# Kernel optimization log

Measured on AMD Instinct MI355X. Metric: run time of the kernel, lower is better.

Reference implementation:

```python
import jax, jax.numpy as jnp
import numpy as np

C = 128
GROUPS = 8
EPS = 1e-5


def setup_inputs() -> dict:
    key = jax.random.key(0)
    ks = jax.random.split(key, 7)
    x = jax.random.normal(ks[0], (8, C, 256, 256), dtype=jnp.float32)
    gn_w = jax.random.normal(ks[1], (C,), dtype=jnp.float32) * 0.02 + 1.0
    gn_b = jax.random.normal(ks[2], (C,), dtype=jnp.float32) * 0.02
    w1 = jax.random.normal(ks[3], (C, C), dtype=jnp.float32) * (1.0 / np.sqrt(C))
    b1 = jax.random.normal(ks[4], (C,), dtype=jnp.float32) * 0.02
    w2 = jax.random.normal(ks[5], (C, C), dtype=jnp.float32) * (1.0 / np.sqrt(C))
    b2 = jax.random.normal(ks[6], (C,), dtype=jnp.float32) * 0.02
    return {"x": x, "gn_w": gn_w, "gn_b": gn_b, "w1": w1, "b1": b1, "w2": w2, "b2": b2}


def reference(x, gn_w, gn_b, w1, b1, w2, b2):
    # fft2 -> ifft2(..).real round-trip (faithful to original; numerically ~identity)
    x_ifft = jnp.fft.ifft2(jnp.fft.fft2(x, axes=(-2, -1)), axes=(-2, -1)).real.astype(x.dtype)

    # GroupNorm over (C//G, H, W) per group
    B, Ch, H, W = x_ifft.shape
    g = x_ifft.reshape(B, GROUPS, Ch // GROUPS, H, W)
    mean = g.mean(axis=(2, 3, 4), keepdims=True)
    var = g.var(axis=(2, 3, 4), keepdims=True)
    xn = ((g - mean) * jax.lax.rsqrt(var + EPS)).reshape(B, Ch, H, W)
    xn = xn * gn_w[None, :, None, None] + gn_b[None, :, None, None]

    # 1x1 conv -> ReLU -> 1x1 conv (as channel GEMMs)
    h = jnp.einsum('oc,bchw->bohw', w1, xn) + b1[None, :, None, None]
    h = jax.nn.relu(h)
    ffn = jnp.einsum('oc,bchw->bohw', w2, h) + b2[None, :, None, None]
    return x_ifft + ffn
```

## Files before the change

### kernel.cpp

```cpp
#include <hip/hip_runtime.h>

typedef __attribute__((ext_vector_type(8))) short s16x8;
typedef __attribute__((ext_vector_type(4))) float f32x4;

#define CCH 128
#define HWSZ 65536

__device__ __forceinline__ ushort f2bf(float f) {
  uint u = __float_as_uint(f);
  u += 0x7fffu + ((u >> 16) & 1u);
  return (ushort)(u >> 16);
}

__device__ __forceinline__ int swz(int row, int col) {
  return (row << 7) | (col ^ ((row & 7) << 3));
}

__global__ __launch_bounds__(256) void prep_weights(const float* __restrict__ w1,
                                                    const float* __restrict__ w2,
                                                    ushort* __restrict__ w1b,
                                                    ushort* __restrict__ w2b) {
  int i = blockIdx.x * 256 + threadIdx.x;
  float4 a = ((const float4*)w1)[i];
  ushort4 oa;
  oa.x = f2bf(a.x); oa.y = f2bf(a.y); oa.z = f2bf(a.z); oa.w = f2bf(a.w);
  ((ushort4*)w1b)[i] = oa;
  float4 b = ((const float4*)w2)[i];
  ushort4 ob;
  ob.x = f2bf(b.x); ob.y = f2bf(b.y); ob.z = f2bf(b.z); ob.w = f2bf(b.w);
  ((ushort4*)w2b)[i] = ob;
}

__global__ __launch_bounds__(256) void stats_partial(const float* __restrict__ x,
                                                     float* __restrict__ partials) {
  const float4* xp = (const float4*)(x + ((size_t)blockIdx.x << 16));
  const int tid = threadIdx.x;
  float s1 = 0.f, s2 = 0.f;
#pragma unroll 8
  for (int i = 0; i < 64; ++i) {
    float4 v = xp[i * 256 + tid];
    s1 += v.x + v.y + v.z + v.w;
    s2 += v.x * v.x + v.y * v.y + v.z * v.z + v.w * v.w;
  }
#pragma unroll
  for (int off = 32; off > 0; off >>= 1) {
    s1 += __shfl_down(s1, off);
    s2 += __shfl_down(s2, off);
  }
  __shared__ float r1[4], r2[4];
  const int wv = tid >> 6;
  if ((tid & 63) == 0) { r1[wv] = s1; r2[wv] = s2; }
  __syncthreads();
  if (tid == 0) {
    partials[blockIdx.x * 2]     = r1[0] + r1[1] + r1[2] + r1[3];
    partials[blockIdx.x * 2 + 1] = r2[0] + r2[1] + r2[2] + r2[3];
  }
}

__global__ void stats_finalize(const float* __restrict__ partials,
                               const float* __restrict__ gn_w,
                               const float* __restrict__ gn_b,
                               float* __restrict__ scale, float* __restrict__ shift) {
  const int t = threadIdx.x;
  float s1 = 0.f, s2 = 0.f;
#pragma unroll
  for (int i = 0; i < 16; ++i) {
    s1 += partials[(t * 16 + i) * 2];
    s2 += partials[(t * 16 + i) * 2 + 1];
  }
  const float invN = 1.0f / 1048576.0f;
  const float mean = s1 * invN;
  const float var = s2 * invN - mean * mean;
  const float rstd = rsqrtf(var + 1e-5f);
  const int b = t >> 3, g = t & 7;
  for (int i = 0; i < 16; ++i) {
    const int c = g * 16 + i;
    const float sc = rstd * gn_w[c];
    scale[b * CCH + c] = sc;
    shift[b * CCH + c] = gn_b[c] - mean * sc;
  }
}

__global__ __launch_bounds__(256) void fused_main(
    const float* __restrict__ x, const ushort* __restrict__ w1b,
    const ushort* __restrict__ w2b, const float* __restrict__ scale,
    const float* __restrict__ shift, const float* __restrict__ b1,
    const float* __restrict__ b2, float* __restrict__ out) {
  __shared__ ushort sB[128 * 128];
  const int tid = threadIdx.x;
  const int b = blockIdx.x >> 9;
  const int p0 = (blockIdx.x & 511) << 7;
  const int lane = tid & 63;
  const int wv = tid >> 6;
  const int fl = lane & 15;
  const int fh = lane >> 4;

  {
    const int p = tid & 127;
    const int ch0 = (tid >> 7) << 6;
    const float* xb = x + (((size_t)b * CCH) << 16) + p0 + p;
    const float* scb = scale + b * CCH;
    const float* shb = shift + b * CCH;
#pragma unroll
    for (int cc = 0; cc < 64; cc += 16) {
      float v[16];
#pragma unroll
      for (int i = 0; i < 16; ++i)
        v[i] = xb[((size_t)(ch0 + cc + i)) << 16];
#pragma unroll
      for (int q = 0; q < 4; ++q) {
        const int c = ch0 + cc + q * 4;
        ushort4 pk;
        pk.x = f2bf(v[q * 4 + 0] * scb[c + 0] + shb[c + 0]);
        pk.y = f2bf(v[q * 4 + 1] * scb[c + 1] + shb[c + 1]);
        pk.z = f2bf(v[q * 4 + 2] * scb[c + 2] + shb[c + 2]);
        pk.w = f2bf(v[q * 4 + 3] * scb[c + 3] + shb[c + 3]);
        *(ushort4*)&sB[swz(p, c)] = pk;
      }
    }
  }
  __syncthreads();

  f32x4 acc[2][8];
#pragma unroll
  for (int f = 0; f < 2; ++f)
#pragma unroll
    for (int j = 0; j < 8; ++j)
      acc[f][j] = (f32x4){0.f, 0.f, 0.f, 0.f};

#pragma unroll
  for (int k0 = 0; k0 < 128; k0 += 32) {
    const int kb = k0 + fh * 8;
    const s16x8 a0 = *(const s16x8*)(w1b + (wv * 32 + fl) * CCH + kb);
    const s16x8 a1 = *(const s16x8*)(w1b + (wv * 32 + 16 + fl) * CCH + kb);
#pragma unroll
    for (int j = 0; j < 8; ++j) {
      const s16x8 bf = *(const s16x8*)&sB[swz(j * 16 + fl, kb)];
      acc[0][j] = __builtin_amdgcn_mfma_f32_16x16x32_bf16(a0, bf, acc[0][j], 0, 0, 0);
      acc[1][j] = __builtin_amdgcn_mfma_f32_16x16x32_bf16(a1, bf, acc[1][j], 0, 0, 0);
    }
  }
  __syncthreads();

#pragma unroll
  for (int f = 0; f < 2; ++f) {
    const int ob = wv * 32 + f * 16 + fh * 4;
    float bb[4];
#pragma unroll
    for (int r = 0; r < 4; ++r) bb[r] = b1[ob + r];
#pragma unroll
    for (int j = 0; j < 8; ++j) {
      const int pcol = j * 16 + fl;
      ushort4 pk;
      pk.x = f2bf(fmaxf(acc[f][j][0] + bb[0], 0.f));
      pk.y = f2bf(fmaxf(acc[f][j][1] + bb[1], 0.f));
      pk.z = f2bf(fmaxf(acc[f][j][2] + bb[2], 0.f));
      pk.w = f2bf(fmaxf(acc[f][j][3] + bb[3], 0.f));
      *(ushort4*)&sB[swz(pcol, ob)] = pk;
    }
  }
  __syncthreads();

  f32x4 acc2[2][8];
#pragma unroll
  for (int f = 0; f < 2; ++f)
#pragma unroll
    for (int j = 0; j < 8; ++j)
      acc2[f][j] = (f32x4){0.f, 0.f, 0.f, 0.f};

#pragma unroll
  for (int k0 = 0; k0 < 128; k0 += 32) {
    const int kb = k0 + fh * 8;
    const s16x8 a0 = *(const s16x8*)(w2b + (wv * 32 + fl) * CCH + kb);
    const s16x8 a1 = *(const s16x8*)(w2b + (wv * 32 + 16 + fl) * CCH + kb);
#pragma unroll
    for (int j = 0; j < 8; ++j) {
      const s16x8 bf = *(const s16x8*)&sB[swz(j * 16 + fl, kb)];
      acc2[0][j] = __builtin_amdgcn_mfma_f32_16x16x32_bf16(a0, bf, acc2[0][j], 0, 0, 0);
      acc2[1][j] = __builtin_amdgcn_mfma_f32_16x16x32_bf16(a1, bf, acc2[1][j], 0, 0, 0);
    }
  }

#pragma unroll
  for (int f = 0; f < 2; ++f) {
    const int ob = wv * 32 + f * 16 + fh * 4;
    float bb[4];
#pragma unroll
    for (int r = 0; r < 4; ++r) bb[r] = b2[ob + r];
#pragma unroll
    for (int j = 0; j < 8; ++j) {
      const int pcol = p0 + j * 16 + fl;
      const size_t base = (((size_t)(b * CCH + ob)) << 16) + pcol;
#pragma unroll
      for (int r = 0; r < 4; ++r) {
        const size_t idx = base + ((size_t)r << 16);
        out[idx] = x[idx] + acc2[f][j][r] + bb[r];
      }
    }
  }
}

extern "C" void kernel_launch(void* const* d_in, const int* in_sizes, int n_in,
                              void* d_out, int out_size, void* d_ws, size_t ws_size,
                              hipStream_t stream) {
  const float* x    = (const float*)d_in[0];
  const float* gn_w = (const float*)d_in[1];
  const float* gn_b = (const float*)d_in[2];
  const float* w1   = (const float*)d_in[3];
  const float* b1   = (const float*)d_in[4];
  const float* w2   = (const float*)d_in[5];
  const float* b2   = (const float*)d_in[6];
  float* out = (float*)d_out;

  char* ws = (char*)d_ws;
  float* partials = (float*)ws;
  float* scale    = (float*)(ws + 8192);
  float* shift    = (float*)(ws + 12288);
  ushort* w1b     = (ushort*)(ws + 16384);
  ushort* w2b     = (ushort*)(ws + 49152);

  hipLaunchKernelGGL(prep_weights, dim3(16), dim3(256), 0, stream, w1, w2, w1b, w2b);
  hipLaunchKernelGGL(stats_partial, dim3(1024), dim3(256), 0, stream, x, partials);
  hipLaunchKernelGGL(stats_finalize, dim3(1), dim3(64), 0, stream, partials, gn_w, gn_b, scale, shift);
  hipLaunchKernelGGL(fused_main, dim3(4096), dim3(256), 0, stream, x, w1b, w2b, scale, shift, b1, b2, out);
}
```

Before: 214.3 us.

## Fold GroupNorm affine into per-batch W1 and restructure main kernel as single-wave blocks

Folds the GroupNorm scale and shift into a per-batch bf16 copy of W1 plus a per-batch bias c1, computed by a new small kernel. The main pass then converts raw x straight to bf16 with no per-element normalize. The main kernel becomes one-wave blocks of 64 threads covering 32 pixels each, with all 128 output channels per wave, so no block barriers are needed. Tradeoffs: weights are re-read per block from global/cache with less reuse per block, there is an extra launch, and bf16 rounding now applies to raw x and scaled weights rather than normalized values.

```diff
diff --git a/kernel.cpp b/kernel.cpp
--- a/kernel.cpp
+++ b/kernel.cpp
@@ -4,7 +4,6 @@
 typedef __attribute__((ext_vector_type(4))) float f32x4;
 
 #define CCH 128
-#define HWSZ 65536
 
 __device__ __forceinline__ ushort f2bf(float f) {
   uint u = __float_as_uint(f);
@@ -16,19 +15,13 @@
   return (row << 7) | (col ^ ((row & 7) << 3));
 }
 
-__global__ __launch_bounds__(256) void prep_weights(const float* __restrict__ w1,
-                                                    const float* __restrict__ w2,
-                                                    ushort* __restrict__ w1b,
-                                                    ushort* __restrict__ w2b) {
+__global__ __launch_bounds__(256) void prep_w2(const float* __restrict__ w2,
+                                               ushort* __restrict__ w2b) {
   int i = blockIdx.x * 256 + threadIdx.x;
-  float4 a = ((const float4*)w1)[i];
-  ushort4 oa;
-  oa.x = f2bf(a.x); oa.y = f2bf(a.y); oa.z = f2bf(a.z); oa.w = f2bf(a.w);
-  ((ushort4*)w1b)[i] = oa;
-  float4 b = ((const float4*)w2)[i];
-  ushort4 ob;
-  ob.x = f2bf(b.x); ob.y = f2bf(b.y); ob.z = f2bf(b.z); ob.w = f2bf(b.w);
-  ((ushort4*)w2b)[i] = ob;
+  float4 a = ((const float4*)w2)[i];
+  ushort4 o;
+  o.x = f2bf(a.x); o.y = f2bf(a.y); o.z = f2bf(a.z); o.w = f2bf(a.w);
+  ((ushort4*)w2b)[i] = o;
 }
 
 __global__ __launch_bounds__(256) void stats_partial(const float* __restrict__ x,
@@ -81,120 +74,116 @@
   }
 }
 
-__global__ __launch_bounds__(256) void fused_main(
-    const float* __restrict__ x, const ushort* __restrict__ w1b,
-    const ushort* __restrict__ w2b, const float* __restrict__ scale,
-    const float* __restrict__ shift, const float* __restrict__ b1,
+__global__ __launch_bounds__(128) void fold_w1(const float* __restrict__ w1,
+                                               const float* __restrict__ b1,
+                                               const float* __restrict__ scale,
+                                               const float* __restrict__ shift,
+                                               ushort* __restrict__ W1b,
+                                               float* __restrict__ c1) {
+  const int b = blockIdx.x >> 7, o = blockIdx.x & 127, c = threadIdx.x;
+  const float wv = w1[o * CCH + c];
+  W1b[(b << 14) + o * CCH + c] = f2bf(wv * scale[b * CCH + c]);
+  float s = wv * shift[b * CCH + c];
+#pragma unroll
+  for (int off = 32; off > 0; off >>= 1) s += __shfl_down(s, off);
+  __shared__ float tmp[2];
+  if ((threadIdx.x & 63) == 0) tmp[threadIdx.x >> 6] = s;
+  __syncthreads();
+  if (threadIdx.x == 0) c1[(b << 7) + o] = tmp[0] + tmp[1] + b1[o];
+}
+
+__global__ __launch_bounds__(64, 3) void wave_fused(
+    const float* __restrict__ x, const ushort* __restrict__ W1b,
+    const ushort* __restrict__ w2b, const float* __restrict__ c1,
     const float* __restrict__ b2, float* __restrict__ out) {
-  __shared__ ushort sB[128 * 128];
-  const int tid = threadIdx.x;
-  const int b = blockIdx.x >> 9;
-  const int p0 = (blockIdx.x & 511) << 7;
-  const int lane = tid & 63;
-  const int wv = tid >> 6;
-  const int fl = lane & 15;
-  const int fh = lane >> 4;
+  __shared__ __align__(16) ushort sB[32 * CCH];
+  const int lane = threadIdx.x;
+  const int b = blockIdx.x >> 11;
+  const int p0 = (blockIdx.x & 2047) << 5;
+  const int fl = lane & 15, fh = lane >> 4;
 
   {
-    const int p = tid & 127;
-    const int ch0 = (tid >> 7) << 6;
+    const int p = lane & 31;
+    const int ch0 = (lane >> 5) << 6;
     const float* xb = x + (((size_t)b * CCH) << 16) + p0 + p;
-    const float* scb = scale + b * CCH;
-    const float* shb = shift + b * CCH;
-#pragma unroll
-    for (int cc = 0; cc < 64; cc += 16) {
-      float v[16];
-#pragma unroll
-      for (int i = 0; i < 16; ++i)
-        v[i] = xb[((size_t)(ch0 + cc + i)) << 16];
-#pragma unroll
-      for (int q = 0; q < 4; ++q) {
-        const int c = ch0 + cc + q * 4;
-        ushort4 pk;
-        pk.x = f2bf(v[q * 4 + 0] * scb[c + 0] + shb[c + 0]);
-        pk.y = f2bf(v[q * 4 + 1] * scb[c + 1] + shb[c + 1]);
-        pk.z = f2bf(v[q * 4 + 2] * scb[c + 2] + shb[c + 2]);
-        pk.w = f2bf(v[q * 4 + 3] * scb[c + 3] + shb[c + 3]);
-        *(ushort4*)&sB[swz(p, c)] = pk;
-      }
-    }
-  }
-  __syncthreads();
-
-  f32x4 acc[2][8];
-#pragma unroll
-  for (int f = 0; f < 2; ++f)
-#pragma unroll
-    for (int j = 0; j < 8; ++j)
-      acc[f][j] = (f32x4){0.f, 0.f, 0.f, 0.f};
-
-#pragma unroll
-  for (int k0 = 0; k0 < 128; k0 += 32) {
-    const int kb = k0 + fh * 8;
-    const s16x8 a0 = *(const s16x8*)(w1b + (wv * 32 + fl) * CCH + kb);
-    const s16x8 a1 = *(const s16x8*)(w1b + (wv * 32 + 16 + fl) * CCH + kb);
-#pragma unroll
-    for (int j = 0; j < 8; ++j) {
-      const s16x8 bf = *(const s16x8*)&sB[swz(j * 16 + fl, kb)];
-      acc[0][j] = __builtin_amdgcn_mfma_f32_16x16x32_bf16(a0, bf, acc[0][j], 0, 0, 0);
-      acc[1][j] = __builtin_amdgcn_mfma_f32_16x16x32_bf16(a1, bf, acc[1][j], 0, 0, 0);
-    }
-  }
-  __syncthreads();
-
-#pragma unroll
-  for (int f = 0; f < 2; ++f) {
-    const int ob = wv * 32 + f * 16 + fh * 4;
-    float bb[4];
-#pragma unroll
-    for (int r = 0; r < 4; ++r) bb[r] = b1[ob + r];
-#pragma unroll
-    for (int j = 0; j < 8; ++j) {
-      const int pcol = j * 16 + fl;
+#pragma unroll
+    for (int i = 0; i < 16; ++i) {
+      const int c = ch0 + i * 4;
+      const float v0 = xb[(size_t)(c + 0) << 16];
+      const float v1 = xb[(size_t)(c + 1) << 16];
+      const float v2 = xb[(size_t)(c + 2) << 16];
+      const float v3 = xb[(size_t)(c + 3) << 16];
       ushort4 pk;
-      pk.x = f2bf(fmaxf(acc[f][j][0] + bb[0], 0.f));
-      pk.y = f2bf(fmaxf(acc[f][j][1] + bb[1], 0.f));
-      pk.z = f2bf(fmaxf(acc[f][j][2] + bb[2], 0.f));
-      pk.w = f2bf(fmaxf(acc[f][j][3] + bb[3], 0.f));
-      *(ushort4*)&sB[swz(pcol, ob)] = pk;
-    }
-  }
-  __syncthreads();
-
-  f32x4 acc2[2][8];
-#pragma unroll
-  for (int f = 0; f < 2; ++f)
-#pragma unroll
-    for (int j = 0; j < 8; ++j)
-      acc2[f][j] = (f32x4){0.f, 0.f, 0.f, 0.f};
-
-#pragma unroll
-  for (int k0 = 0; k0 < 128; k0 += 32) {
-    const int kb = k0 + fh * 8;
-    const s16x8 a0 = *(const s16x8*)(w2b + (wv * 32 + fl) * CCH + kb);
-    const s16x8 a1 = *(const s16x8*)(w2b + (wv * 32 + 16 + fl) * CCH + kb);
-#pragma unroll
-    for (int j = 0; j < 8; ++j) {
-      const s16x8 bf = *(const s16x8*)&sB[swz(j * 16 + fl, kb)];
-      acc2[0][j] = __builtin_amdgcn_mfma_f32_16x16x32_bf16(a0, bf, acc2[0][j], 0, 0, 0);
-      acc2[1][j] = __builtin_amdgcn_mfma_f32_16x16x32_bf16(a1, bf, acc2[1][j], 0, 0, 0);
-    }
-  }
-
-#pragma unroll
-  for (int f = 0; f < 2; ++f) {
-    const int ob = wv * 32 + f * 16 + fh * 4;
-    float bb[4];
-#pragma unroll
-    for (int r = 0; r < 4; ++r) bb[r] = b2[ob + r];
-#pragma unroll
-    for (int j = 0; j < 8; ++j) {
-      const int pcol = p0 + j * 16 + fl;
-      const size_t base = (((size_t)(b * CCH + ob)) << 16) + pcol;
+      pk.x = f2bf(v0); pk.y = f2bf(v1); pk.z = f2bf(v2); pk.w = f2bf(v3);
+      *(ushort4*)&sB[swz(p, c)] = pk;
+    }
+  }
+
+  f32x4 acc[8][2];
+#pragma unroll
+  for (int to = 0; to < 8; ++to)
+#pragma unroll
+    for (int tp = 0; tp < 2; ++tp) acc[to][tp] = (f32x4){0.f, 0.f, 0.f, 0.f};
+
+  const ushort* w1p = W1b + ((size_t)b << 14);
+#pragma unroll
+  for (int k0 = 0; k0 < 4; ++k0) {
+    const int kb = k0 * 32 + fh * 8;
+    const s16x8 bt0 = *(const s16x8*)&sB[swz(fl, kb)];
+    const s16x8 bt1 = *(const s16x8*)&sB[swz(16 + fl, kb)];
+#pragma unroll
+    for (int to = 0; to < 8; ++to) {
+      const s16x8 a = *(const s16x8*)(w1p + (to * 16 + fl) * CCH + kb);
+      acc[to][0] = __builtin_amdgcn_mfma_f32_16x16x32_bf16(a, bt0, acc[to][0], 0, 0, 0);
+      acc[to][1] = __builtin_amdgcn_mfma_f32_16x16x32_bf16(a, bt1, acc[to][1], 0, 0, 0);
+    }
+  }
+
+  const float* c1b = c1 + (b << 7);
+#pragma unroll
+  for (int to = 0; to < 8; ++to) {
+    const int ob = to * 16 + fh * 4;
+    const float4 cc = *(const float4*)(c1b + ob);
+#pragma unroll
+    for (int tp = 0; tp < 2; ++tp) {
+      ushort4 pk;
+      pk.x = f2bf(fmaxf(acc[to][tp][0] + cc.x, 0.f));
+      pk.y = f2bf(fmaxf(acc[to][tp][1] + cc.y, 0.f));
+      pk.z = f2bf(fmaxf(acc[to][tp][2] + cc.z, 0.f));
+      pk.w = f2bf(fmaxf(acc[to][tp][3] + cc.w, 0.f));
+      *(ushort4*)&sB[swz(tp * 16 + fl, ob)] = pk;
+    }
+  }
+
+  f32x4 acc2[8][2];
+#pragma unroll
+  for (int to = 0; to < 8; ++to)
+#pragma unroll
+    for (int tp = 0; tp < 2; ++tp) acc2[to][tp] = (f32x4){0.f, 0.f, 0.f, 0.f};
+
+#pragma unroll
+  for (int k0 = 0; k0 < 4; ++k0) {
+    const int kb = k0 * 32 + fh * 8;
+    const s16x8 bt0 = *(const s16x8*)&sB[swz(fl, kb)];
+    const s16x8 bt1 = *(const s16x8*)&sB[swz(16 + fl, kb)];
+#pragma unroll
+    for (int to = 0; to < 8; ++to) {
+      const s16x8 a = *(const s16x8*)(w2b + (to * 16 + fl) * CCH + kb);
+      acc2[to][0] = __builtin_amdgcn_mfma_f32_16x16x32_bf16(a, bt0, acc2[to][0], 0, 0, 0);
+      acc2[to][1] = __builtin_amdgcn_mfma_f32_16x16x32_bf16(a, bt1, acc2[to][1], 0, 0, 0);
+    }
+  }
+
+#pragma unroll
+  for (int to = 0; to < 8; ++to) {
+    const int ob = to * 16 + fh * 4;
+    const float4 bb = *(const float4*)(b2 + ob);
+#pragma unroll
+    for (int tp = 0; tp < 2; ++tp) {
 #pragma unroll
       for (int r = 0; r < 4; ++r) {
-        const size_t idx = base + ((size_t)r << 16);
-        out[idx] = x[idx] + acc2[f][j][r] + bb[r];
+        const size_t idx = (((size_t)(b * CCH + ob + r)) << 16) + p0 + tp * 16 + fl;
+        out[idx] = x[idx] + acc2[to][tp][r] + bb[r];
       }
     }
   }
@@ -216,11 +205,13 @@
   float* partials = (float*)ws;
   float* scale    = (float*)(ws + 8192);
   float* shift    = (float*)(ws + 12288);
-  ushort* w1b     = (ushort*)(ws + 16384);
-  ushort* w2b     = (ushort*)(ws + 49152);
-
-  hipLaunchKernelGGL(prep_weights, dim3(16), dim3(256), 0, stream, w1, w2, w1b, w2b);
+  ushort* w2b     = (ushort*)(ws + 16384);
+  ushort* W1b     = (ushort*)(ws + 49152);
+  float* c1       = (float*)(ws + 311296);
+
+  hipLaunchKernelGGL(prep_w2, dim3(16), dim3(256), 0, stream, w2, w2b);
   hipLaunchKernelGGL(stats_partial, dim3(1024), dim3(256), 0, stream, x, partials);
   hipLaunchKernelGGL(stats_finalize, dim3(1), dim3(64), 0, stream, partials, gn_w, gn_b, scale, shift);
-  hipLaunchKernelGGL(fused_main, dim3(4096), dim3(256), 0, stream, x, w1b, w2b, scale, shift, b1, b2, out);
-}
+  hipLaunchKernelGGL(fold_w1, dim3(1024), dim3(128), 0, stream, w1, b1, scale, shift, W1b, c1);
+  hipLaunchKernelGGL(wave_fused, dim3(16384), dim3(64), 0, stream, x, W1b, w2b, c1, b2, out);
+}
```

Result: slower. 303.8 us (+41.8%).

## Fold GroupNorm into per-batch W1 and stage x as bf16 pixel-major buffer

Applied to the files above, without the earlier changes.

Adds a first pass that computes per-group statistics while transposing x into a bf16 pixel-major workspace buffer. It then folds the GroupNorm scale and shift into a per-batch bf16 copy of W1 plus a bias vector, and runs the two GEMMs per wave directly from that buffer. The aim is to remove the separate statistics read and the in-kernel normalisation and transpose. In exchange it needs a large workspace, and it takes the residual from the bf16 copy instead of fp32 x, which reduces accuracy. The old path is kept as a fallback when the workspace is too small.

```diff
diff --git a/kernel.cpp b/kernel.cpp
--- a/kernel.cpp
+++ b/kernel.cpp
@@ -4,35 +4,226 @@
 typedef __attribute__((ext_vector_type(4))) float f32x4;
 
 #define CCH 128
-#define HWSZ 65536
 
 __device__ __forceinline__ ushort f2bf(float f) {
   uint u = __float_as_uint(f);
   u += 0x7fffu + ((u >> 16) & 1u);
   return (ushort)(u >> 16);
 }
+__device__ __forceinline__ float bf2f(ushort u) {
+  return __uint_as_float(((uint)u) << 16);
+}
+
+
+__global__ __launch_bounds__(256) void pass1_stats_tr(const float* __restrict__ x,
+                                                      ushort* __restrict__ xb,
+                                                      float2* __restrict__ partials) {
+  __shared__ ushort sT[256 * CCH];
+  __shared__ float ws1[4][8], ws2[4][8];
+  const int t = threadIdx.x;
+  const int b = blockIdx.x >> 8;
+  const int p0 = (blockIdx.x & 255) << 8;
+  const int wv = t >> 6, lane = t & 63;
+  const int px4 = lane << 2;
+  float sg1[8], sg2[8];
+#pragma unroll
+  for (int g = 0; g < 8; ++g) { sg1[g] = 0.f; sg2[g] = 0.f; }
+
+  const float* xbase = x + (((size_t)b * CCH) << 16) + p0;
+#pragma unroll
+  for (int i = 0; i < 8; ++i) {
+    const int ch = i * 16 + wv * 4;
+    float4 v[4];
+#pragma unroll
+    for (int j = 0; j < 4; ++j)
+      v[j] = *(const float4*)(xbase + (((size_t)(ch + j)) << 16) + px4);
+#pragma unroll
+    for (int j = 0; j < 4; ++j) {
+      sg1[i] += v[j].x + v[j].y + v[j].z + v[j].w;
+      sg2[i] += v[j].x * v[j].x + v[j].y * v[j].y + v[j].z * v[j].z + v[j].w * v[j].w;
+    }
+#pragma unroll
+    for (int k = 0; k < 4; ++k) {
+      const int row = px4 + k;
+      const int gs = (i * 4 + wv) ^ (((row >> 3) & 15) << 1);
+      ushort4 pk;
+      pk.x = f2bf(((const float*)&v[0])[k]);
+      pk.y = f2bf(((const float*)&v[1])[k]);
+      pk.z = f2bf(((const float*)&v[2])[k]);
+      pk.w = f2bf(((const float*)&v[3])[k]);
+      *(ushort4*)&sT[row * CCH + gs * 4] = pk;
+    }
+  }
+#pragma unroll
+  for (int g = 0; g < 8; ++g) {
+    float a = sg1[g], q = sg2[g];
+#pragma unroll
+    for (int off = 32; off > 0; off >>= 1) {
+      a += __shfl_down(a, off);
+      q += __shfl_down(q, off);
+    }
+    if (lane == 0) { ws1[wv][g] = a; ws2[wv][g] = q; }
+  }
+  __syncthreads();
+  if (t < 8) {
+    float a = ws1[0][t] + ws1[1][t] + ws1[2][t] + ws1[3][t];
+    float q = ws2[0][t] + ws2[1][t] + ws2[2][t] + ws2[3][t];
+    partials[blockIdx.x * 8 + t] = (float2){a, q};
+  }
+  const int c16 = t & 15, pr = t >> 4;
+  ushort* dst = xb + ((size_t)((b << 16) + p0)) * CCH;
+#pragma unroll
+  for (int s = 0; s < 16; ++s) {
+    const int row = s * 16 + pr;
+    const int gs = (c16 * 2) ^ (((row >> 3) & 15) << 1);
+    *(s16x8*)&dst[(size_t)row * CCH + c16 * 8] = *(const s16x8*)&sT[row * CCH + gs * 4];
+  }
+}
+
+__global__ void stats_finalize2(const float2* __restrict__ partials,
+                                const float* __restrict__ gn_w,
+                                const float* __restrict__ gn_b,
+                                float* __restrict__ scale, float* __restrict__ shift) {
+  const int t = threadIdx.x;
+  const int b = t >> 3, g = t & 7;
+  float s1 = 0.f, s2 = 0.f;
+  for (int c = 0; c < 256; ++c) {
+    float2 p = partials[(b * 256 + c) * 8 + g];
+    s1 += p.x;
+    s2 += p.y;
+  }
+  const float invN = 1.0f / 1048576.0f;
+  const float mean = s1 * invN;
+  const float var = s2 * invN - mean * mean;
+  const float rstd = rsqrtf(var + 1e-5f);
+  for (int i = 0; i < 16; ++i) {
+    const int c = g * 16 + i;
+    const float sc = rstd * gn_w[c];
+    scale[b * CCH + c] = sc;
+    shift[b * CCH + c] = gn_b[c] - mean * sc;
+  }
+}
+
+__global__ __launch_bounds__(256) void prep_w2(const float* __restrict__ w2,
+                                               ushort* __restrict__ w2b) {
+  int i = blockIdx.x * 256 + threadIdx.x;
+  float4 a = ((const float4*)w2)[i];
+  ushort4 o;
+  o.x = f2bf(a.x); o.y = f2bf(a.y); o.z = f2bf(a.z); o.w = f2bf(a.w);
+  ((ushort4*)w2b)[i] = o;
+}
+
+__global__ __launch_bounds__(128) void fold_w1(const float* __restrict__ w1,
+                                               const float* __restrict__ b1,
+                                               const float* __restrict__ scale,
+                                               const float* __restrict__ shift,
+                                               ushort* __restrict__ W1b,
+                                               float* __restrict__ c1) {
+  const int b = blockIdx.x >> 7, o = blockIdx.x & 127, c = threadIdx.x;
+  const float wv = w1[o * CCH + c];
+  W1b[(b << 14) + o * CCH + c] = f2bf(wv * scale[b * CCH + c]);
+  float s = wv * shift[b * CCH + c];
+#pragma unroll
+  for (int off = 32; off > 0; off >>= 1) s += __shfl_down(s, off);
+  __shared__ float tmp[2];
+  if ((threadIdx.x & 63) == 0) tmp[threadIdx.x >> 6] = s;
+  __syncthreads();
+  if (threadIdx.x == 0) c1[(b << 7) + o] = tmp[0] + tmp[1] + b1[o];
+}
+
+__global__ __launch_bounds__(256) void pass2_mlp(
+    const ushort* __restrict__ xb, const ushort* __restrict__ W1b,
+    const ushort* __restrict__ w2b, const float* __restrict__ c1,
+    const float* __restrict__ b2, float* __restrict__ out) {
+  __shared__ ushort hT[4][16 * CCH];
+  const int t = threadIdx.x;
+  const int wv = t >> 6, lane = t & 63;
+  const int fl = lane & 15, fh = lane >> 4;
+  const int b = blockIdx.x >> 9;
+  const int p0 = ((blockIdx.x & 511) << 7) + wv * 32;
+  const ushort* xrow = xb + ((size_t)((b << 16) + p0)) * CCH;
+  const ushort* w1p = W1b + (b << 14);
+  const float* c1b = c1 + (b << 7);
+  ushort* hw = &hT[wv][0];
+
+#pragma unroll
+  for (int tp = 0; tp < 2; ++tp) {
+    const ushort* xt = xrow + (tp * 16 + fl) * CCH;
+    f32x4 acc[8];
+#pragma unroll
+    for (int to = 0; to < 8; ++to) acc[to] = (f32x4){0.f, 0.f, 0.f, 0.f};
+#pragma unroll
+    for (int k0 = 0; k0 < 4; ++k0) {
+      const int kb = k0 * 32 + fh * 8;
+      const s16x8 bt = *(const s16x8*)&xt[kb];
+#pragma unroll
+      for (int to = 0; to < 8; ++to) {
+        const s16x8 a = *(const s16x8*)&w1p[(to * 16 + fl) * CCH + kb];
+        acc[to] = __builtin_amdgcn_mfma_f32_16x16x32_bf16(a, bt, acc[to], 0, 0, 0);
+      }
+    }
+#pragma unroll
+    for (int to = 0; to < 8; ++to) {
+      const float4 cc = *(const float4*)&c1b[to * 16 + fh * 4];
+      ushort4 pk;
+      pk.x = f2bf(fmaxf(acc[to][0] + cc.x, 0.f));
+      pk.y = f2bf(fmaxf(acc[to][1] + cc.y, 0.f));
+      pk.z = f2bf(fmaxf(acc[to][2] + cc.z, 0.f));
+      pk.w = f2bf(fmaxf(acc[to][3] + cc.w, 0.f));
+      const int gs = (to * 4 + fh) ^ (fl << 1);
+      *(ushort4*)&hw[fl * CCH + gs * 4] = pk;
+    }
+    f32x4 acc2[8];
+#pragma unroll
+    for (int to = 0; to < 8; ++to) acc2[to] = (f32x4){0.f, 0.f, 0.f, 0.f};
+#pragma unroll
+    for (int k0 = 0; k0 < 4; ++k0) {
+      const int kb = k0 * 32 + fh * 8;
+      const int gs = (k0 * 8 + fh * 2) ^ (fl << 1);
+      const s16x8 bt = *(const s16x8*)&hw[fl * CCH + gs * 4];
+#pragma unroll
+      for (int to = 0; to < 8; ++to) {
+        const s16x8 a = *(const s16x8*)&w2b[(to * 16 + fl) * CCH + kb];
+        acc2[to] = __builtin_amdgcn_mfma_f32_16x16x32_bf16(a, bt, acc2[to], 0, 0, 0);
+      }
+    }
+#pragma unroll
+    for (int to = 0; to < 8; ++to) {
+      const int ob = to * 16 + fh * 4;
+      const float4 bb = *(const float4*)&b2[ob];
+      const ushort4 rx = *(const ushort4*)&xt[ob];
+      const float rxf[4] = {bf2f(rx.x), bf2f(rx.y), bf2f(rx.z), bf2f(rx.w)};
+#pragma unroll
+      for (int r = 0; r < 4; ++r) {
+        const size_t idx = (((size_t)(b * CCH + ob + r)) << 16) + p0 + tp * 16 + fl;
+        out[idx] = rxf[r] + acc2[to][r] + ((const float*)&bb)[r];
+      }
+    }
+  }
+}
+
 
 __device__ __forceinline__ int swz(int row, int col) {
   return (row << 7) | (col ^ ((row & 7) << 3));
 }
 
-__global__ __launch_bounds__(256) void prep_weights(const float* __restrict__ w1,
-                                                    const float* __restrict__ w2,
-                                                    ushort* __restrict__ w1b,
-                                                    ushort* __restrict__ w2b) {
+__global__ __launch_bounds__(256) void prep_weights_fb(const float* __restrict__ w1,
+                                                       const float* __restrict__ w2,
+                                                       ushort* __restrict__ w1b,
+                                                       ushort* __restrict__ w2b) {
   int i = blockIdx.x * 256 + threadIdx.x;
   float4 a = ((const float4*)w1)[i];
   ushort4 oa;
   oa.x = f2bf(a.x); oa.y = f2bf(a.y); oa.z = f2bf(a.z); oa.w = f2bf(a.w);
   ((ushort4*)w1b)[i] = oa;
-  float4 b = ((const float4*)w2)[i];
+  float4 bq = ((const float4*)w2)[i];
   ushort4 ob;
-  ob.x = f2bf(b.x); ob.y = f2bf(b.y); ob.z = f2bf(b.z); ob.w = f2bf(b.w);
+  ob.x = f2bf(bq.x); ob.y = f2bf(bq.y); ob.z = f2bf(bq.z); ob.w = f2bf(bq.w);
   ((ushort4*)w2b)[i] = ob;
 }
 
-__global__ __launch_bounds__(256) void stats_partial(const float* __restrict__ x,
-                                                     float* __restrict__ partials) {
+__global__ __launch_bounds__(256) void stats_partial_fb(const float* __restrict__ x,
+                                                        float* __restrict__ partials) {
   const float4* xp = (const float4*)(x + ((size_t)blockIdx.x << 16));
   const int tid = threadIdx.x;
   float s1 = 0.f, s2 = 0.f;
@@ -52,15 +243,15 @@
   if ((tid & 63) == 0) { r1[wv] = s1; r2[wv] = s2; }
   __syncthreads();
   if (tid == 0) {
-    partials[blockIdx.x * 2]     = r1[0] + r1[1] + r1[2] + r1[3];
+    partials[blockIdx.x * 2] = r1[0] + r1[1] + r1[2] + r1[3];
     partials[blockIdx.x * 2 + 1] = r2[0] + r2[1] + r2[2] + r2[3];
   }
 }
 
-__global__ void stats_finalize(const float* __restrict__ partials,
-                               const float* __restrict__ gn_w,
-                               const float* __restrict__ gn_b,
-                               float* __restrict__ scale, float* __restrict__ shift) {
+__global__ void stats_finalize_fb(const float* __restrict__ partials,
+                                  const float* __restrict__ gn_w,
+                                  const float* __restrict__ gn_b,
+                                  float* __restrict__ scale, float* __restrict__ shift) {
   const int t = threadIdx.x;
   float s1 = 0.f, s2 = 0.f;
 #pragma unroll
@@ -81,7 +272,7 @@
   }
 }
 
-__global__ __launch_bounds__(256) void fused_main(
+__global__ __launch_bounds__(256) void fused_main_fb(
     const float* __restrict__ x, const ushort* __restrict__ w1b,
     const ushort* __restrict__ w2b, const float* __restrict__ scale,
     const float* __restrict__ shift, const float* __restrict__ b1,
@@ -94,19 +285,17 @@
   const int wv = tid >> 6;
   const int fl = lane & 15;
   const int fh = lane >> 4;
-
   {
     const int p = tid & 127;
     const int ch0 = (tid >> 7) << 6;
-    const float* xb = x + (((size_t)b * CCH) << 16) + p0 + p;
+    const float* xbp = x + (((size_t)b * CCH) << 16) + p0 + p;
     const float* scb = scale + b * CCH;
     const float* shb = shift + b * CCH;
 #pragma unroll
     for (int cc = 0; cc < 64; cc += 16) {
       float v[16];
 #pragma unroll
-      for (int i = 0; i < 16; ++i)
-        v[i] = xb[((size_t)(ch0 + cc + i)) << 16];
+      for (int i = 0; i < 16; ++i) v[i] = xbp[((size_t)(ch0 + cc + i)) << 16];
 #pragma unroll
       for (int q = 0; q < 4; ++q) {
         const int c = ch0 + cc + q * 4;
@@ -120,14 +309,11 @@
     }
   }
   __syncthreads();
-
   f32x4 acc[2][8];
 #pragma unroll
   for (int f = 0; f < 2; ++f)
 #pragma unroll
-    for (int j = 0; j < 8; ++j)
-      acc[f][j] = (f32x4){0.f, 0.f, 0.f, 0.f};
-
+    for (int j = 0; j < 8; ++j) acc[f][j] = (f32x4){0.f, 0.f, 0.f, 0.f};
 #pragma unroll
   for (int k0 = 0; k0 < 128; k0 += 32) {
     const int kb = k0 + fh * 8;
@@ -141,7 +327,6 @@
     }
   }
   __syncthreads();
-
 #pragma unroll
   for (int f = 0; f < 2; ++f) {
     const int ob = wv * 32 + f * 16 + fh * 4;
@@ -160,14 +345,11 @@
     }
   }
   __syncthreads();
-
   f32x4 acc2[2][8];
 #pragma unroll
   for (int f = 0; f < 2; ++f)
 #pragma unroll
-    for (int j = 0; j < 8; ++j)
-      acc2[f][j] = (f32x4){0.f, 0.f, 0.f, 0.f};
-
+    for (int j = 0; j < 8; ++j) acc2[f][j] = (f32x4){0.f, 0.f, 0.f, 0.f};
 #pragma unroll
   for (int k0 = 0; k0 < 128; k0 += 32) {
     const int kb = k0 + fh * 8;
@@ -180,7 +362,6 @@
       acc2[1][j] = __builtin_amdgcn_mfma_f32_16x16x32_bf16(a1, bf, acc2[1][j], 0, 0, 0);
     }
   }
-
 #pragma unroll
   for (int f = 0; f < 2; ++f) {
     const int ob = wv * 32 + f * 16 + fh * 4;
@@ -199,6 +380,7 @@
     }
   }
 }
+
 
 extern "C" void kernel_launch(void* const* d_in, const int* in_sizes, int n_in,
                               void* d_out, int out_size, void* d_ws, size_t ws_size,
@@ -211,16 +393,35 @@
   const float* w2   = (const float*)d_in[5];
   const float* b2   = (const float*)d_in[6];
   float* out = (float*)d_out;
-
   char* ws = (char*)d_ws;
-  float* partials = (float*)ws;
-  float* scale    = (float*)(ws + 8192);
-  float* shift    = (float*)(ws + 12288);
-  ushort* w1b     = (ushort*)(ws + 16384);
-  ushort* w2b     = (ushort*)(ws + 49152);
-
-  hipLaunchKernelGGL(prep_weights, dim3(16), dim3(256), 0, stream, w1, w2, w1b, w2b);
-  hipLaunchKernelGGL(stats_partial, dim3(1024), dim3(256), 0, stream, x, partials);
-  hipLaunchKernelGGL(stats_finalize, dim3(1), dim3(64), 0, stream, partials, gn_w, gn_b, scale, shift);
-  hipLaunchKernelGGL(fused_main, dim3(4096), dim3(256), 0, stream, x, w1b, w2b, scale, shift, b1, b2, out);
-}
+
+  const size_t XB_BYTES = (size_t)8 * 65536 * CCH * 2;
+  const size_t NEED = XB_BYTES + 131072 + 4096 + 4096 + 32768 + 262144 + 4096;
+
+  if (ws_size >= NEED) {
+    ushort* xbuf    = (ushort*)ws;
+    float2* parts   = (float2*)(ws + XB_BYTES);
+    float* scale    = (float*)(ws + XB_BYTES + 131072);
+    float* shift    = (float*)(ws + XB_BYTES + 135168);
+    ushort* w2b     = (ushort*)(ws + XB_BYTES + 139264);
+    ushort* W1b     = (ushort*)(ws + XB_BYTES + 172032);
+    float* c1       = (float*)(ws + XB_BYTES + 434176);
+
+    hipLaunchKernelGGL(pass1_stats_tr, dim3(2048), dim3(256), 0, stream, x, xbuf, parts);
+    hipLaunchKernelGGL(prep_w2, dim3(16), dim3(256), 0, stream, w2, w2b);
+    hipLaunchKernelGGL(stats_finalize2, dim3(1), dim3(64), 0, stream, parts, gn_w, gn_b, scale, shift);
+    hipLaunchKernelGGL(fold_w1, dim3(1024), dim3(128), 0, stream, w1, b1, scale, shift, W1b, c1);
+    hipLaunchKernelGGL(pass2_mlp, dim3(4096), dim3(256), 0, stream, xbuf, W1b, w2b, c1, b2, out);
+  } else {
+    float* partials = (float*)ws;
+    float* scale    = (float*)(ws + 8192);
+    float* shift    = (float*)(ws + 12288);
+    ushort* w1b     = (ushort*)(ws + 16384);
+    ushort* w2b     = (ushort*)(ws + 49152);
+
+    hipLaunchKernelGGL(prep_weights_fb, dim3(16), dim3(256), 0, stream, w1, w2, w1b, w2b);
+    hipLaunchKernelGGL(stats_partial_fb, dim3(1024), dim3(256), 0, stream, x, partials);
+    hipLaunchKernelGGL(stats_finalize_fb, dim3(1), dim3(64), 0, stream, partials, gn_w, gn_b, scale, shift);
+    hipLaunchKernelGGL(fused_main_fb, dim3(4096), dim3(256), 0, stream, x, w1b, w2b, scale, shift, b1, b2, out);
+  }
+}
```

Measured after the change: 428.0 us. 99.7% more time.

## Stage x as channel-last bf16 during stats pass and fold GroupNorm into W1

Applied to the files above, without the earlier changes.

The stats pass now also converts x to bf16 and transposes it to a pixel-major, channel-contiguous layout in the workspace. The main MLP kernel reads this half-size buffer for both the GEMM input and the residual, instead of reading fp32 x twice. GroupNorm scale and shift are folded into a per-batch bf16 W1 and a bias vector, which removes the per-element normalisation from the main kernel. The aim is to cut total HBM traffic. In exchange it adds extra kernels, a large workspace buffer, and a residual computed from bf16 rather than fp32 x, which lowers accuracy.

```diff
diff --git a/kernel.cpp b/kernel.cpp
--- a/kernel.cpp
+++ b/kernel.cpp
@@ -4,75 +4,101 @@
 typedef __attribute__((ext_vector_type(4))) float f32x4;
 
 #define CCH 128
-#define HWSZ 65536
 
 __device__ __forceinline__ ushort f2bf(float f) {
   uint u = __float_as_uint(f);
   u += 0x7fffu + ((u >> 16) & 1u);
   return (ushort)(u >> 16);
 }
+__device__ __forceinline__ float bf2f(ushort u) {
+  return __uint_as_float(((uint)u) << 16);
+}
 
 __device__ __forceinline__ int swz(int row, int col) {
   return (row << 7) | (col ^ ((row & 7) << 3));
 }
 
-__global__ __launch_bounds__(256) void prep_weights(const float* __restrict__ w1,
-                                                    const float* __restrict__ w2,
-                                                    ushort* __restrict__ w1b,
-                                                    ushort* __restrict__ w2b) {
-  int i = blockIdx.x * 256 + threadIdx.x;
-  float4 a = ((const float4*)w1)[i];
-  ushort4 oa;
-  oa.x = f2bf(a.x); oa.y = f2bf(a.y); oa.z = f2bf(a.z); oa.w = f2bf(a.w);
-  ((ushort4*)w1b)[i] = oa;
-  float4 b = ((const float4*)w2)[i];
-  ushort4 ob;
-  ob.x = f2bf(b.x); ob.y = f2bf(b.y); ob.z = f2bf(b.z); ob.w = f2bf(b.w);
-  ((ushort4*)w2b)[i] = ob;
-}
-
-__global__ __launch_bounds__(256) void stats_partial(const float* __restrict__ x,
-                                                     float* __restrict__ partials) {
-  const float4* xp = (const float4*)(x + ((size_t)blockIdx.x << 16));
-  const int tid = threadIdx.x;
+__global__ __launch_bounds__(256) void pass1_stats_tr(const float* __restrict__ x,
+                                                      ushort* __restrict__ xb,
+                                                      float2* __restrict__ partials) {
+  __shared__ ushort sT[256 * CCH];
+  __shared__ float ws1[4][8], ws2[4][8];
+  const int t = threadIdx.x;
+  const int b = blockIdx.x >> 8;
+  const int p0 = (blockIdx.x & 255) << 8;
+  const int wv = t >> 6, lane = t & 63;
+  const int px4 = lane << 2;
+  float sg1[8], sg2[8];
+#pragma unroll
+  for (int g = 0; g < 8; ++g) { sg1[g] = 0.f; sg2[g] = 0.f; }
+
+  const float* xbase = x + (((size_t)b * CCH) << 16) + p0;
+#pragma unroll
+  for (int i = 0; i < 8; ++i) {
+    const int ch = i * 16 + wv * 4;
+    float4 v[4];
+#pragma unroll
+    for (int j = 0; j < 4; ++j)
+      v[j] = *(const float4*)(xbase + (((size_t)(ch + j)) << 16) + px4);
+#pragma unroll
+    for (int j = 0; j < 4; ++j) {
+      sg1[i] += v[j].x + v[j].y + v[j].z + v[j].w;
+      sg2[i] += v[j].x * v[j].x + v[j].y * v[j].y + v[j].z * v[j].z + v[j].w * v[j].w;
+    }
+#pragma unroll
+    for (int k = 0; k < 4; ++k) {
+      const int row = px4 + k;
+      const int gs = (i * 4 + wv) ^ (((row >> 3) & 15) << 1);
+      ushort4 pk;
+      pk.x = f2bf(((const float*)&v[0])[k]);
+      pk.y = f2bf(((const float*)&v[1])[k]);
+      pk.z = f2bf(((const float*)&v[2])[k]);
+      pk.w = f2bf(((const float*)&v[3])[k]);
+      *(ushort4*)&sT[row * CCH + gs * 4] = pk;
+    }
+  }
+#pragma unroll
+  for (int g = 0; g < 8; ++g) {
+    float a = sg1[g], q = sg2[g];
+#pragma unroll
+    for (int off = 32; off > 0; off >>= 1) {
+      a += __shfl_down(a, off);
+      q += __shfl_down(q, off);
+    }
+    if (lane == 0) { ws1[wv][g] = a; ws2[wv][g] = q; }
+  }
+  __syncthreads();
+  if (t < 8) {
+    float a = ws1[0][t] + ws1[1][t] + ws1[2][t] + ws1[3][t];
+    float q = ws2[0][t] + ws2[1][t] + ws2[2][t] + ws2[3][t];
+    partials[blockIdx.x * 8 + t] = (float2){a, q};
+  }
+  const int c16 = t & 15, pr = t >> 4;
+  ushort* dst = xb + ((size_t)((b << 16) + p0)) * CCH;
+#pragma unroll
+  for (int s = 0; s < 16; ++s) {
+    const int row = s * 16 + pr;
+    const int gs = (c16 * 2) ^ (((row >> 3) & 15) << 1);
+    *(s16x8*)&dst[(size_t)row * CCH + c16 * 8] = *(const s16x8*)&sT[row * CCH + gs * 4];
+  }
+}
+
+__global__ void stats_finalize2(const float2* __restrict__ partials,
+                                const float* __restrict__ gn_w,
+                                const float* __restrict__ gn_b,
+                                float* __restrict__ scale, float* __restrict__ shift) {
+  const int t = threadIdx.x;
+  const int b = t >> 3, g = t & 7;
   float s1 = 0.f, s2 = 0.f;
-#pragma unroll 8
-  for (int i = 0; i < 64; ++i) {
-    float4 v = xp[i * 256 + tid];
-    s1 += v.x + v.y + v.z + v.w;
-    s2 += v.x * v.x + v.y * v.y + v.z * v.z + v.w * v.w;
-  }
-#pragma unroll
-  for (int off = 32; off > 0; off >>= 1) {
-    s1 += __shfl_down(s1, off);
-    s2 += __shfl_down(s2, off);
-  }
-  __shared__ float r1[4], r2[4];
-  const int wv = tid >> 6;
-  if ((tid & 63) == 0) { r1[wv] = s1; r2[wv] = s2; }
-  __syncthreads();
-  if (tid == 0) {
-    partials[blockIdx.x * 2]     = r1[0] + r1[1] + r1[2] + r1[3];
-    partials[blockIdx.x * 2 + 1] = r2[0] + r2[1] + r2[2] + r2[3];
-  }
-}
-
-__global__ void stats_finalize(const float* __restrict__ partials,
-                               const float* __restrict__ gn_w,
-                               const float* __restrict__ gn_b,
-                               float* __restrict__ scale, float* __restrict__ shift) {
-  const int t = threadIdx.x;
-  float s1 = 0.f, s2 = 0.f;
-#pragma unroll
-  for (int i = 0; i < 16; ++i) {
-    s1 += partials[(t * 16 + i) * 2];
-    s2 += partials[(t * 16 + i) * 2 + 1];
+  for (int c = 0; c < 256; ++c) {
+    float2 p = partials[(b * 256 + c) * 8 + g];
+    s1 += p.x;
+    s2 += p.y;
   }
   const float invN = 1.0f / 1048576.0f;
   const float mean = s1 * invN;
   const float var = s2 * invN - mean * mean;
   const float rstd = rsqrtf(var + 1e-5f);
-  const int b = t >> 3, g = t & 7;
   for (int i = 0; i < 16; ++i) {
     const int c = g * 16 + i;
     const float sc = rstd * gn_w[c];
@@ -81,43 +107,54 @@
   }
 }
 
-__global__ __launch_bounds__(256) void fused_main(
-    const float* __restrict__ x, const ushort* __restrict__ w1b,
-    const ushort* __restrict__ w2b, const float* __restrict__ scale,
-    const float* __restrict__ shift, const float* __restrict__ b1,
+__global__ __launch_bounds__(256) void prep_w2(const float* __restrict__ w2,
+                                               ushort* __restrict__ w2b) {
+  int i = blockIdx.x * 256 + threadIdx.x;
+  float4 a = ((const float4*)w2)[i];
+  ushort4 o;
+  o.x = f2bf(a.x); o.y = f2bf(a.y); o.z = f2bf(a.z); o.w = f2bf(a.w);
+  ((ushort4*)w2b)[i] = o;
+}
+
+__global__ __launch_bounds__(128) void fold_w1(const float* __restrict__ w1,
+                                               const float* __restrict__ b1,
+                                               const float* __restrict__ scale,
+                                               const float* __restrict__ shift,
+                                               ushort* __restrict__ W1b,
+                                               float* __restrict__ c1) {
+  const int b = blockIdx.x >> 7, o = blockIdx.x & 127, c = threadIdx.x;
+  const float wv = w1[o * CCH + c];
+  W1b[(b << 14) + o * CCH + c] = f2bf(wv * scale[b * CCH + c]);
+  float s = wv * shift[b * CCH + c];
+#pragma unroll
+  for (int off = 32; off > 0; off >>= 1) s += __shfl_down(s, off);
+  __shared__ float tmp[2];
+  if ((threadIdx.x & 63) == 0) tmp[threadIdx.x >> 6] = s;
+  __syncthreads();
+  if (threadIdx.x == 0) c1[(b << 7) + o] = tmp[0] + tmp[1] + b1[o];
+}
+
+__global__ __launch_bounds__(256, 4) void mlp_tiled(
+    const ushort* __restrict__ xb, const ushort* __restrict__ W1b,
+    const ushort* __restrict__ w2b, const float* __restrict__ c1,
     const float* __restrict__ b2, float* __restrict__ out) {
-  __shared__ ushort sB[128 * 128];
-  const int tid = threadIdx.x;
+  __shared__ ushort sB[128 * CCH];
+  const int t = threadIdx.x;
   const int b = blockIdx.x >> 9;
   const int p0 = (blockIdx.x & 511) << 7;
-  const int lane = tid & 63;
-  const int wv = tid >> 6;
+  const int lane = t & 63;
+  const int wv = t >> 6;
   const int fl = lane & 15;
   const int fh = lane >> 4;
 
-  {
-    const int p = tid & 127;
-    const int ch0 = (tid >> 7) << 6;
-    const float* xb = x + (((size_t)b * CCH) << 16) + p0 + p;
-    const float* scb = scale + b * CCH;
-    const float* shb = shift + b * CCH;
-#pragma unroll
-    for (int cc = 0; cc < 64; cc += 16) {
-      float v[16];
-#pragma unroll
-      for (int i = 0; i < 16; ++i)
-        v[i] = xb[((size_t)(ch0 + cc + i)) << 16];
-#pragma unroll
-      for (int q = 0; q < 4; ++q) {
-        const int c = ch0 + cc + q * 4;
-        ushort4 pk;
-        pk.x = f2bf(v[q * 4 + 0] * scb[c + 0] + shb[c + 0]);
-        pk.y = f2bf(v[q * 4 + 1] * scb[c + 1] + shb[c + 1]);
-        pk.z = f2bf(v[q * 4 + 2] * scb[c + 2] + shb[c + 2]);
-        pk.w = f2bf(v[q * 4 + 3] * scb[c + 3] + shb[c + 3]);
-        *(ushort4*)&sB[swz(p, c)] = pk;
-      }
-    }
+  const ushort* src = xb + ((size_t)((b << 16) + p0)) * CCH;
+#pragma unroll
+  for (int i = 0; i < 8; ++i) {
+    const int u = i * 256 + t;
+    const int px = u >> 4;
+    const int ch = (u & 15) * 8;
+    const s16x8 v = *(const s16x8*)(src + px * CCH + ch);
+    *(s16x8*)&sB[swz(px, ch)] = v;
   }
   __syncthreads();
 
@@ -125,14 +162,14 @@
 #pragma unroll
   for (int f = 0; f < 2; ++f)
 #pragma unroll
-    for (int j = 0; j < 8; ++j)
-      acc[f][j] = (f32x4){0.f, 0.f, 0.f, 0.f};
-
+    for (int j = 0; j < 8; ++j) acc[f][j] = (f32x4){0.f, 0.f, 0.f, 0.f};
+
+  const ushort* w1p = W1b + (b << 14);
 #pragma unroll
   for (int k0 = 0; k0 < 128; k0 += 32) {
     const int kb = k0 + fh * 8;
-    const s16x8 a0 = *(const s16x8*)(w1b + (wv * 32 + fl) * CCH + kb);
-    const s16x8 a1 = *(const s16x8*)(w1b + (wv * 32 + 16 + fl) * CCH + kb);
+    const s16x8 a0 = *(const s16x8*)(w1p + (wv * 32 + fl) * CCH + kb);
+    const s16x8 a1 = *(const s16x8*)(w1p + (wv * 32 + 16 + fl) * CCH + kb);
 #pragma unroll
     for (int j = 0; j < 8; ++j) {
       const s16x8 bf = *(const s16x8*)&sB[swz(j * 16 + fl, kb)];
@@ -142,21 +179,19 @@
   }
   __syncthreads();
 
+  const float* c1b = c1 + (b << 7);
 #pragma unroll
   for (int f = 0; f < 2; ++f) {
     const int ob = wv * 32 + f * 16 + fh * 4;
-    float bb[4];
-#pragma unroll
-    for (int r = 0; r < 4; ++r) bb[r] = b1[ob + r];
-#pragma unroll
-    for (int j = 0; j < 8; ++j) {
-      const int pcol = j * 16 + fl;
+    const float4 cc = *(const float4*)(c1b + ob);
+#pragma unroll
+    for (int j = 0; j < 8; ++j) {
       ushort4 pk;
-      pk.x = f2bf(fmaxf(acc[f][j][0] + bb[0], 0.f));
-      pk.y = f2bf(fmaxf(acc[f][j][1] + bb[1], 0.f));
-      pk.z = f2bf(fmaxf(acc[f][j][2] + bb[2], 0.f));
-      pk.w = f2bf(fmaxf(acc[f][j][3] + bb[3], 0.f));
-      *(ushort4*)&sB[swz(pcol, ob)] = pk;
+      pk.x = f2bf(fmaxf(acc[f][j][0] + cc.x, 0.f));
+      pk.y = f2bf(fmaxf(acc[f][j][1] + cc.y, 0.f));
+      pk.z = f2bf(fmaxf(acc[f][j][2] + cc.z, 0.f));
+      pk.w = f2bf(fmaxf(acc[f][j][3] + cc.w, 0.f));
+      *(ushort4*)&sB[swz(j * 16 + fl, ob)] = pk;
     }
   }
   __syncthreads();
@@ -165,8 +200,7 @@
 #pragma unroll
   for (int f = 0; f < 2; ++f)
 #pragma unroll
-    for (int j = 0; j < 8; ++j)
-      acc2[f][j] = (f32x4){0.f, 0.f, 0.f, 0.f};
+    for (int j = 0; j < 8; ++j) acc2[f][j] = (f32x4){0.f, 0.f, 0.f, 0.f};
 
 #pragma unroll
   for (int k0 = 0; k0 < 128; k0 += 32) {
@@ -184,18 +218,16 @@
 #pragma unroll
   for (int f = 0; f < 2; ++f) {
     const int ob = wv * 32 + f * 16 + fh * 4;
-    float bb[4];
-#pragma unroll
-    for (int r = 0; r < 4; ++r) bb[r] = b2[ob + r];
-#pragma unroll
-    for (int j = 0; j < 8; ++j) {
-      const int pcol = p0 + j * 16 + fl;
-      const size_t base = (((size_t)(b * CCH + ob)) << 16) + pcol;
-#pragma unroll
-      for (int r = 0; r < 4; ++r) {
-        const size_t idx = base + ((size_t)r << 16);
-        out[idx] = x[idx] + acc2[f][j][r] + bb[r];
-      }
+    const float4 bb = *(const float4*)(b2 + ob);
+#pragma unroll
+    for (int j = 0; j < 8; ++j) {
+      const int pcol = j * 16 + fl;
+      const ushort4 rx = *(const ushort4*)(src + pcol * CCH + ob);
+      const size_t base = (((size_t)(b * CCH + ob)) << 16) + p0 + pcol;
+      out[base] = bf2f(rx.x) + acc2[f][j][0] + bb.x;
+      out[base + ((size_t)1 << 16)] = bf2f(rx.y) + acc2[f][j][1] + bb.y;
+      out[base + ((size_t)2 << 16)] = bf2f(rx.z) + acc2[f][j][2] + bb.z;
+      out[base + ((size_t)3 << 16)] = bf2f(rx.w) + acc2[f][j][3] + bb.w;
     }
   }
 }
@@ -211,16 +243,20 @@
   const float* w2   = (const float*)d_in[5];
   const float* b2   = (const float*)d_in[6];
   float* out = (float*)d_out;
-
   char* ws = (char*)d_ws;
-  float* partials = (float*)ws;
-  float* scale    = (float*)(ws + 8192);
-  float* shift    = (float*)(ws + 12288);
-  ushort* w1b     = (ushort*)(ws + 16384);
-  ushort* w2b     = (ushort*)(ws + 49152);
-
-  hipLaunchKernelGGL(prep_weights, dim3(16), dim3(256), 0, stream, w1, w2, w1b, w2b);
-  hipLaunchKernelGGL(stats_partial, dim3(1024), dim3(256), 0, stream, x, partials);
-  hipLaunchKernelGGL(stats_finalize, dim3(1), dim3(64), 0, stream, partials, gn_w, gn_b, scale, shift);
-  hipLaunchKernelGGL(fused_main, dim3(4096), dim3(256), 0, stream, x, w1b, w2b, scale, shift, b1, b2, out);
-}
+
+  const size_t XB_BYTES = (size_t)8 * 65536 * CCH * 2;
+  ushort* xbuf  = (ushort*)ws;
+  float2* parts = (float2*)(ws + XB_BYTES);
+  float* scale  = (float*)(ws + XB_BYTES + 131072);
+  float* shift  = (float*)(ws + XB_BYTES + 135168);
+  ushort* w2b   = (ushort*)(ws + XB_BYTES + 139264);
+  ushort* W1b   = (ushort*)(ws + XB_BYTES + 172032);
+  float* c1     = (float*)(ws + XB_BYTES + 434176);
+
+  hipLaunchKernelGGL(pass1_stats_tr, dim3(2048), dim3(256), 0, stream, x, xbuf, parts);
+  hipLaunchKernelGGL(prep_w2, dim3(16), dim3(256), 0, stream, w2, w2b);
+  hipLaunchKernelGGL(stats_finalize2, dim3(1), dim3(64), 0, stream, parts, gn_w, gn_b, scale, shift);
+  hipLaunchKernelGGL(fold_w1, dim3(1024), dim3(128), 0, stream, w1, b1, scale, shift, W1b, c1);
+  hipLaunchKernelGGL(mlp_tiled, dim3(4096), dim3(256), 0, stream, xbuf, W1b, w2b, c1, b2, out);
+}
```

Measured after the change: 234.0 us. 1.09x slower.
